# Kernel optimization log

Measured on AMD Instinct MI355X. Metric: run time of the kernel, lower is better.

The kernel has to match this reference:

```python
import jax, jax.numpy as jnp
import numpy as np

N_NODES = 100000
N_EDGES = 800000
N_GRAPHS = 64
N_ETYPES = 4
D = 150
HID = 512
PASSES = 5


def setup_inputs() -> dict:
    key = jax.random.key(0)
    ks = jax.random.split(key, 16)
    s = 0.1
    return {
        "nodes": jax.random.normal(ks[0], (N_NODES, D), jnp.float32),
        "problem_class": jax.random.normal(ks[1], (N_GRAPHS, 1), jnp.float32),
        "edge_src": jax.random.randint(ks[2], (N_EDGES,), 0, N_NODES, jnp.int32),
        "edge_dst": jax.random.randint(ks[3], (N_EDGES,), 0, N_NODES, jnp.int32),
        "edge_type": jax.random.randint(ks[4], (N_EDGES,), 0, N_ETYPES, jnp.int32),
        "graph_ids": jnp.sort(jax.random.randint(ks[5], (N_NODES,), 0, N_GRAPHS, jnp.int32)),
        "W_e": jax.random.normal(ks[6], (N_ETYPES, D, D), jnp.float32) * s,
        "b_e": jax.random.normal(ks[7], (N_ETYPES, D), jnp.float32) * s,
        "w_ih": jax.random.normal(ks[8], (3 * D, D), jnp.float32) * s,
        "w_hh": jax.random.normal(ks[9], (3 * D, D), jnp.float32) * s,
        "b_ih": jax.random.normal(ks[10], (3 * D,), jnp.float32) * s,
        "b_hh": jax.random.normal(ks[11], (3 * D,), jnp.float32) * s,
        "fc1_w": jax.random.normal(ks[12], (D + 1, HID), jnp.float32) * s,
        "fc1_b": jax.random.normal(ks[13], (HID,), jnp.float32) * s,
        "fc2_w": jax.random.normal(ks[14], (HID, 10), jnp.float32) * s,
        "fc2_b": jax.random.normal(ks[15], (10,), jnp.float32) * s,
    }


def _gru_cell(x, h, w_ih, w_hh, b_ih, b_hh):
    # torch.nn.GRUCell math, gate order (r, z, n)
    gi = x @ w_ih.T + b_ih
    gh = h @ w_hh.T + b_hh
    i_r, i_z, i_n = jnp.split(gi, 3, axis=1)
    h_r, h_z, h_n = jnp.split(gh, 3, axis=1)
    r = jax.nn.sigmoid(i_r + h_r)
    z = jax.nn.sigmoid(i_z + h_z)
    n = jnp.tanh(i_n + r * h_n)
    return (1.0 - z) * n + z * h


def reference(nodes, problem_class, edge_src, edge_dst, edge_type, graph_ids,
              W_e, b_e, w_ih, w_hh, b_ih, b_hh, fc1_w, fc1_b, fc2_w, fc2_b):
    n_nodes = nodes.shape[0]
    n_graphs = problem_class.shape[0]
    n_types = W_e.shape[0]

    # in-degree per edge type (for the per-edge Linear bias contribution)
    type_onehot = jax.nn.one_hot(edge_type, n_types, dtype=nodes.dtype)  # [E, T]
    deg = jax.ops.segment_sum(type_onehot, edge_dst, num_segments=n_nodes)  # [N, T]
    bias_inc = deg @ b_e  # [N, D] = sum_t deg_t * b_t

    h = nodes
    for _ in range(PASSES):
        h_src = h[edge_src]  # [E, D] gather
        inc = bias_inc
        for t in range(n_types):
            # aggregate first, apply the edge-type Linear after (linearity)
            agg = jax.ops.segment_sum(
                jnp.where((edge_type == t)[:, None], h_src, 0.0),
                edge_dst, num_segments=n_nodes)  # [N, D]
            inc = inc + agg @ W_e[t].T
        h = _gru_cell(inc, h, w_ih, w_hh, b_ih, b_hh)

    # graph readout: sum nodes, log, nan -> 0, relu
    g = jax.ops.segment_sum(h, graph_ids, num_segments=n_graphs)  # [B, D]
    l = jnp.log(g)
    l = jax.nn.relu(jnp.where(jnp.isnan(l), 0.0, l))
    x = jnp.concatenate([l, problem_class], axis=1)  # [B, D+1]
    x = jax.nn.leaky_relu(x @ fc1_w + fc1_b)
    return x @ fc2_w + fc2_b
```

## Files before the change

kernel.cpp:

```cpp
#include <hip/hip_runtime.h>
#include <hip/hip_bf16.h>
#include <cstdint>
#include <cstddef>

#define NN 100000
#define NE 800000
#define NG 64
#define NT 4
#define DD 150
#define HS 160
#define HIDN 512
#define NPASS 5
#define NBINS (NN*NT)
#define RPB 16

typedef short  s8v  __attribute__((ext_vector_type(8)));
typedef float  f32x4 __attribute__((ext_vector_type(4)));

static __device__ __forceinline__ float sigmoidf_(float x){ return 1.f/(1.f+expf(-x)); }
static __device__ __forceinline__ short f2bf(float x){
  __hip_bfloat16 b = __float2bfloat16(x);
  return *(short*)&b;
}
static __device__ __forceinline__ float bf2f(short s){
  union { unsigned u; float f; } v; v.u = ((unsigned)(unsigned short)s) << 16; return v.f;
}
static __device__ __forceinline__ void split_bf(float x, short& hi, short& lo){
  hi = f2bf(x);
  lo = f2bf(x - bf2f(hi));
}


__global__ void count_kernel(const int* __restrict__ dst, const int* __restrict__ typ,
                             unsigned* __restrict__ deg){
  int e = blockIdx.x*256 + threadIdx.x;
  if (e < NE) atomicAdd(&deg[dst[e]*NT + typ[e]], 1u);
}

__device__ unsigned block_excl_base(unsigned threadSum){
  const int tid = threadIdx.x;
  const int lane = tid & 63, wid = tid >> 6;
  unsigned s = threadSum;
  #pragma unroll
  for (int d = 1; d < 64; d <<= 1){ unsigned t = __shfl_up(s, d); if (lane >= d) s += t; }
  __shared__ unsigned wsum[4];
  if (lane == 63) wsum[wid] = s;
  __syncthreads();
  unsigned base = 0;
  for (int w = 0; w < wid; w++) base += wsum[w];
  return base + s - threadSum;
}

__global__ void scan_reduce(const unsigned* __restrict__ deg, unsigned* __restrict__ bsum){
  const int base = blockIdx.x*1024 + threadIdx.x*4;
  unsigned s = 0;
  #pragma unroll
  for (int i = 0; i < 4; i++){ const int idx = base+i; if (idx < NBINS) s += deg[idx]; }
  #pragma unroll
  for (int d = 1; d < 64; d <<= 1) s += __shfl_down(s, d);
  __shared__ unsigned ws4[4];
  const int lane = threadIdx.x & 63, wid = threadIdx.x >> 6;
  if (lane == 0) ws4[wid] = s;
  __syncthreads();
  if (threadIdx.x == 0) bsum[blockIdx.x] = ws4[0]+ws4[1]+ws4[2]+ws4[3];
}

__global__ void scan_block(unsigned* bsum, int n){
  const int tid = threadIdx.x;
  unsigned v[4]; unsigned s = 0;
  #pragma unroll
  for (int i = 0; i < 4; i++){ const int idx = tid*4+i; v[i] = (idx < n) ? bsum[idx] : 0u; s += v[i]; }
  unsigned run = block_excl_base(s);
  #pragma unroll
  for (int i = 0; i < 4; i++){ const int idx = tid*4+i; if (idx < n) bsum[idx] = run; run += v[i]; }
}

__global__ void scan_final(const unsigned* __restrict__ deg, const unsigned* __restrict__ bsum,
                           unsigned* __restrict__ off){
  const int tid = threadIdx.x;
  const int base0 = blockIdx.x*1024 + tid*4;
  unsigned v[4]; unsigned s = 0;
  #pragma unroll
  for (int i = 0; i < 4; i++){ const int idx = base0+i; v[i] = (idx < NBINS) ? deg[idx] : 0u; s += v[i]; }
  unsigned run = block_excl_base(s) + bsum[blockIdx.x];
  #pragma unroll
  for (int i = 0; i < 4; i++){ const int idx = base0+i; if (idx < NBINS) off[idx] = run; run += v[i]; }
  if (blockIdx.x == 0 && tid == 0) off[NBINS] = NE;
}

__global__ void scatter_sort(const int* __restrict__ src, const int* __restrict__ dst,
                             const int* __restrict__ typ, unsigned* __restrict__ cur,
                             int* __restrict__ srcSorted){
  int e = blockIdx.x*256 + threadIdx.x;
  if (e < NE){
    const int bin = dst[e]*NT + typ[e];
    const unsigned p = atomicAdd(&cur[bin], 1u);
    srcSorted[p] = src[e];
  }
}

__global__ void init_h(const float* __restrict__ nodes, float* __restrict__ h0){
  const long long idx = (long long)blockIdx.x*256 + threadIdx.x;
  if (idx >= (long long)NN*HS) return;
  const int row = (int)(idx / HS), col = (int)(idx % HS);
  float v = 0.f;
  if (col < DD) v = nodes[(size_t)row*DD + col];
  h0[idx] = v;
}

__global__ void build_bfrag_msg(const float* __restrict__ W, unsigned short* __restrict__ out){
  const int idx = blockIdx.x*256 + threadIdx.x;
  if (idx >= NT*5*10*2*512) return;
  const int w = idx & 511;
  int r = idx >> 9;
  const int c = r % 2;  r /= 2;
  const int i = r % 10; r /= 10;
  const int s = r % 5;  const int t = r / 5;
  const int l = w >> 3, j = w & 7;
  const int n  = 16*i + (l & 15);
  const int kk = 32*s + (l >> 4)*8 + j;
  float v = 0.f;
  if (n < DD && kk < DD) v = W[(size_t)(t*DD + n)*DD + kk];
  short hi, lo; split_bf(v, hi, lo);
  out[(size_t)((t*5 + s)*20 + i*2 + c)*512 + w] = (unsigned short)(c ? lo : hi);
}

__global__ void build_bfrag_gru(const float* __restrict__ w_ih, const float* __restrict__ w_hh,
                                unsigned short* __restrict__ out){
  const int idx = blockIdx.x*256 + threadIdx.x;
  if (idx >= 10*3*2*2*5*512) return;
  const int w = idx & 511;
  int r = idx >> 9;
  const int s = r % 5;    r /= 5;
  const int c = r % 2;    r /= 2;
  const int u = r % 2;    r /= 2;
  const int part = r % 3; const int iT = r / 3;
  const int P = part*2 + u;
  const int g = P >> 1;
  const float* W = (P & 1) ? w_hh : w_ih;
  const int l = w >> 3, j = w & 7;
  const int n  = 16*iT + (l & 15);
  const int kk = 32*s + (l >> 4)*8 + j;
  float v = 0.f;
  if (n < DD && kk < DD) v = W[(size_t)(g*DD + n)*DD + kk];
  short hi, lo; split_bf(v, hi, lo);
  out[(size_t)((iT*3 + part)*20 + u*10 + c*5 + s)*512 + w] = (unsigned short)(c ? lo : hi);
}

#define MFMA3(acc, ahi, alo, bhi, blo) \
  acc = __builtin_amdgcn_mfma_f32_16x16x32_bf16(ahi, bhi, acc, 0,0,0); \
  acc = __builtin_amdgcn_mfma_f32_16x16x32_bf16(alo, bhi, acc, 0,0,0); \
  acc = __builtin_amdgcn_mfma_f32_16x16x32_bf16(ahi, blo, acc, 0,0,0);

__global__ __launch_bounds__(256, 2) void msg_kernel(
    const float* __restrict__ h, const int* __restrict__ srcS,
    const unsigned* __restrict__ off, const unsigned* __restrict__ deg,
    const float* __restrict__ b_e,
    const unsigned short* __restrict__ BfE2,
    float* __restrict__ inc)
{
  __shared__ short Bs[2][20*512];
  const int tid = threadIdx.x, wave = tid >> 6, l = tid & 63;
  const int m = l & 15, q = l >> 4, q8 = q*8;
  const int arow = blockIdx.x*64 + wave*16 + m;
  const bool av = (arow < NN);
  const int lb8 = l*8;

  f32x4 acc[10];
  #pragma unroll
  for (int i = 0; i < 10; i++) acc[i] = (f32x4)(0.0f);

  #pragma unroll
  for (int k2 = 0; k2 < 5; k2++){
    const int c = tid + k2*256;
    *(s8v*)(&Bs[0][c*8]) = *(const s8v*)(BfE2 + (size_t)c*8);
  }
  __syncthreads();

  s8v sv[5];
  for (int t = 0; t < NT; t++){
    #pragma unroll
    for (int k2 = 0; k2 < 5; k2++){
      const int c = tid + k2*256;
      sv[k2] = *(const s8v*)(BfE2 + (size_t)(t*5 + 1)*10240 + (size_t)c*8);
    }

    float a[5][8];
    #pragma unroll
    for (int s = 0; s < 5; s++)
      #pragma unroll
      for (int j = 0; j < 8; j++) a[s][j] = 0.f;

    int lo = 0, hi = 0;
    if (av){ const int bin = arow*NT + t; lo = (int)off[bin]; hi = (int)off[bin+1]; }
    int e = lo;
    int i0 = (e   < hi) ? srcS[e]   : 0;
    int i1 = (e+1 < hi) ? srcS[e+1] : -1;
    while (e < hi){
      const int n0 = (e+2 < hi) ? srcS[e+2] : 0;
      const int n1 = (e+3 < hi) ? srcS[e+3] : -1;
      const float* p0 = h + (size_t)i0*HS + q8;
      const float* p1 = h + (size_t)(i1 < 0 ? 0 : i1)*HS + q8;
      const float w1 = (i1 < 0) ? 0.f : 1.f;
      f32x4 v[10], u[10];
      #pragma unroll
      for (int s = 0; s < 5; s++){
        v[2*s]   = *(const f32x4*)(p0 + 32*s);
        v[2*s+1] = *(const f32x4*)(p0 + 32*s + 4);
      }
      #pragma unroll
      for (int s = 0; s < 5; s++){
        u[2*s]   = *(const f32x4*)(p1 + 32*s);
        u[2*s+1] = *(const f32x4*)(p1 + 32*s + 4);
      }
      #pragma unroll
      for (int s = 0; s < 5; s++){
        #pragma unroll
        for (int j = 0; j < 4; j++){
          a[s][j]   += v[2*s][j];
          a[s][j]   = fmaf(w1, u[2*s][j], a[s][j]);
          a[s][4+j] += v[2*s+1][j];
          a[s][4+j] = fmaf(w1, u[2*s+1][j], a[s][4+j]);
        }
      }
      e += 2; i0 = n0; i1 = n1;
    }

    s8v af_hi[5], af_lo[5];
    #pragma unroll
    for (int s = 0; s < 5; s++)
      #pragma unroll
      for (int j = 0; j < 8; j++){
        short h2, l2; split_bf(a[s][j], h2, l2);
        af_hi[s][j] = h2; af_lo[s][j] = l2;
      }

    #pragma unroll
    for (int st = 0; st < 5; st++){
      const int sidx = t*5 + st;
      const short* bsr = &Bs[sidx & 1][0];
      #pragma unroll
      for (int i = 0; i < 10; i++){
        const s8v bh = *(const s8v*)(bsr + (i*2+0)*512 + lb8);
        const s8v bl = *(const s8v*)(bsr + (i*2+1)*512 + lb8);
        MFMA3(acc[i], af_hi[st], af_lo[st], bh, bl)
      }
      if (sidx + 1 < 20){
        short* bsw = &Bs[(sidx+1) & 1][0];
        #pragma unroll
        for (int k2 = 0; k2 < 5; k2++){
          const int c = tid + k2*256;
          *(s8v*)(bsw + c*8) = sv[k2];
        }
      }
      if (st < 4 && sidx + 2 < 20){
        #pragma unroll
        for (int k2 = 0; k2 < 5; k2++){
          const int c = tid + k2*256;
          sv[k2] = *(const s8v*)(BfE2 + (size_t)(sidx+2)*10240 + (size_t)c*8);
        }
      }
      __syncthreads();
    }
  }

  const int crow0 = blockIdx.x*64 + wave*16 + q*4;
  #pragma unroll
  for (int r = 0; r < 4; r++){
    const int crow = crow0 + r;
    if (crow < NN){
      const uint4 dg = *(const uint4*)(&deg[crow*NT]);
      const float d0=(float)dg.x, d1=(float)dg.y, d2=(float)dg.z, d3=(float)dg.w;
      float* op = inc + (size_t)crow*HS;
      #pragma unroll
      for (int i = 0; i < 10; i++){
        const int c = 16*i + m;
        float val = 0.f;
        if (c < DD)
          val = acc[i][r] + fmaf(d0, b_e[c], fmaf(d1, b_e[DD+c],
                  fmaf(d2, b_e[2*DD+c], d3*b_e[3*DD+c])));
        op[c] = val;
      }
    }
  }
}

__global__ __launch_bounds__(512, 2) void gru_kernel(
    const float* __restrict__ h, float* __restrict__ incnext,
    const unsigned short* __restrict__ BfG,
    const float* __restrict__ b_ih, const float* __restrict__ b_hh)
{
  __shared__ short Bs[2][20*512];
  const int tid = threadIdx.x, wave = tid >> 6, l = tid & 63;
  const int m = l & 15, q = l >> 4, q8 = q*8;
  const int arow = blockIdx.x*128 + wave*16 + m;
  const bool av = (arow < NN);
  const int lb8 = l*8;
  const int crow0 = blockIdx.x*128 + wave*16 + q*4;

  s8v afi_h[5], afi_l[5], afh_h[5], afh_l[5];
  {
    const float* ip = incnext + (size_t)(av ? arow : 0)*HS;
    const float* hp = h       + (size_t)(av ? arow : 0)*HS;
    #pragma unroll
    for (int s = 0; s < 5; s++){
      const int b = 32*s + q8;
      const f32x4 x0 = *(const f32x4*)(ip + b), x1 = *(const f32x4*)(ip + b + 4);
      const f32x4 y0 = *(const f32x4*)(hp + b), y1 = *(const f32x4*)(hp + b + 4);
      #pragma unroll
      for (int j = 0; j < 4; j++){
        short h2, l2;
        split_bf(x0[j], h2, l2); afi_h[s][j]   = h2; afi_l[s][j]   = l2;
        split_bf(x1[j], h2, l2); afi_h[s][4+j] = h2; afi_l[s][4+j] = l2;
        split_bf(y0[j], h2, l2); afh_h[s][j]   = h2; afh_l[s][j]   = l2;
        split_bf(y1[j], h2, l2); afh_h[s][4+j] = h2; afh_l[s][4+j] = l2;
      }
    }
  }

  #pragma unroll
  for (int k2 = 0; k2 < 3; k2++){
    const int c = tid + k2*512;
    if (c < 1280) *(s8v*)(&Bs[0][c*8]) = *(const s8v*)(BfG + (size_t)c*8);
  }
  __syncthreads();

  s8v sv[3];
  #pragma unroll
  for (int k2 = 0; k2 < 3; k2++){
    const int c = tid + k2*512;
    if (c < 1280) sv[k2] = *(const s8v*)(BfG + (size_t)10240 + (size_t)c*8);
  }

  f32x4 aR=(f32x4)(0.f), aZ=(f32x4)(0.f), aIN=(f32x4)(0.f), aHN=(f32x4)(0.f);
  float hv[4] = {0.f,0.f,0.f,0.f};

  for (int k = 0; k < 30; k++){
    const int iT = k/3, part = k - 3*iT;
    const int d = 16*iT + m;
    if (part == 0){
      aR = (f32x4)(0.f); aZ = (f32x4)(0.f); aIN = (f32x4)(0.f); aHN = (f32x4)(0.f);
      #pragma unroll
      for (int r = 0; r < 4; r++){
        hv[r] = 0.f;
        if (crow0 + r < NN && d < DD) hv[r] = h[(size_t)(crow0+r)*HS + d];
      }
    }

    const short* bsr = &Bs[k & 1][0];
    #pragma unroll
    for (int s = 0; s < 5; s++){
      const s8v b0h = *(const s8v*)(bsr + (     s)*512 + lb8);
      const s8v b0l = *(const s8v*)(bsr + ( 5 + s)*512 + lb8);
      const s8v b1h = *(const s8v*)(bsr + (10 + s)*512 + lb8);
      const s8v b1l = *(const s8v*)(bsr + (15 + s)*512 + lb8);
      if (part == 0){
        MFMA3(aR, afi_h[s], afi_l[s], b0h, b0l)
        MFMA3(aR, afh_h[s], afh_l[s], b1h, b1l)
      } else if (part == 1){
        MFMA3(aZ, afi_h[s], afi_l[s], b0h, b0l)
        MFMA3(aZ, afh_h[s], afh_l[s], b1h, b1l)
      } else {
        MFMA3(aIN, afi_h[s], afi_l[s], b0h, b0l)
        MFMA3(aHN, afh_h[s], afh_l[s], b1h, b1l)
      }
    }

    if (k < 29){
      short* bsw = &Bs[(k+1) & 1][0];
      #pragma unroll
      for (int k2 = 0; k2 < 3; k2++){
        const int c = tid + k2*512;
        if (c < 1280) *(s8v*)(bsw + c*8) = sv[k2];
      }
    }
    if (k < 28){
      #pragma unroll
      for (int k2 = 0; k2 < 3; k2++){
        const int c = tid + k2*512;
        if (c < 1280) sv[k2] = *(const s8v*)(BfG + (size_t)(k+2)*10240 + (size_t)c*8);
      }
    }

    if (part == 2 && d < DD){
      const float br   = b_ih[d]    + b_hh[d];
      const float bz   = b_ih[DD+d] + b_hh[DD+d];
      const float bin2 = b_ih[2*DD+d];
      const float bhn  = b_hh[2*DD+d];
      #pragma unroll
      for (int r = 0; r < 4; r++){
        const int crow = crow0 + r;
        if (crow < NN){
          const float rr = sigmoidf_(aR[r] + br);
          const float zz = sigmoidf_(aZ[r] + bz);
          const float nn = tanhf(aIN[r] + bin2 + rr*(aHN[r] + bhn));
          incnext[(size_t)crow*HS + d] = (1.f - zz)*nn + zz*hv[r];
        }
      }
    }
    __syncthreads();
  }
}

__global__ void readout1(const float* __restrict__ h, const int* __restrict__ gids,
                         float* __restrict__ part){
  const int g = blockIdx.x >> 4, s = blockIdx.x & (RPB-1);
  const int tid = threadIdx.x;
  __shared__ int sb[2];
  if (tid < 2){
    const int target = g + tid;
    int lo = 0, hi = NN;
    while (lo < hi){ const int mid = (lo+hi) >> 1; if (gids[mid] < target) lo = mid+1; else hi = mid; }
    sb[tid] = lo;
  }
  __syncthreads();
  const int lo = sb[0], hi = sb[1];
  const int len = hi - lo;
  const int per = (len + RPB - 1) / RPB;
  const int nlo = lo + s*per;
  const int nhi = (nlo + per < hi) ? (nlo + per) : hi;
  if (tid < DD){
    float acc = 0.f;
    for (int n = nlo; n < nhi; n++) acc += h[(size_t)n*HS + tid];
    part[(size_t)blockIdx.x*DD + tid] = acc;
  }
}

__global__ void readout2(const float* __restrict__ part, const float* __restrict__ pclass,
                         float* __restrict__ xbuf){
  const int g = blockIdx.x, tid = threadIdx.x;
  if (tid < DD){
    float acc = 0.f;
    #pragma unroll
    for (int s = 0; s < RPB; s++) acc += part[(size_t)(g*RPB + s)*DD + tid];
    float l = logf(acc);
    if (isnan(l)) l = 0.f;
    l = fmaxf(l, 0.f);
    xbuf[g*(DD+1)+tid] = l;
  }
  if (tid == DD) xbuf[g*(DD+1)+DD] = pclass[g];
}

__global__ void fc1_kernel(const float* __restrict__ xbuf, const float* __restrict__ w,
                           const float* __restrict__ b, float* __restrict__ hid){
  const int g = blockIdx.x, tid = threadIdx.x;
  __shared__ float xs[DD+1];
  if (tid < DD+1) xs[tid] = xbuf[g*(DD+1)+tid];
  __syncthreads();
  float acc = b[tid];
  for (int k = 0; k < DD+1; k++) acc = fmaf(xs[k], w[k*HIDN + tid], acc);
  hid[g*HIDN + tid] = (acc > 0.f) ? acc : 0.01f*acc;
}

__global__ void fc2_kernel(const float* __restrict__ hid, const float* __restrict__ w,
                           const float* __restrict__ b, float* __restrict__ out){
  const int g = blockIdx.x, tid = threadIdx.x;
  __shared__ float hs[HIDN];
  for (int i = tid; i < HIDN; i += 64) hs[i] = hid[g*HIDN + i];
  __syncthreads();
  if (tid < 10){
    float acc = b[tid];
    for (int k = 0; k < HIDN; k++) acc = fmaf(hs[k], w[k*10 + tid], acc);
    out[g*10 + tid] = acc;
  }
}

extern "C" void kernel_launch(void* const* d_in, const int* in_sizes, int n_in,
                              void* d_out, int out_size, void* d_ws, size_t ws_size,
                              hipStream_t stream)
{
  (void)in_sizes; (void)n_in; (void)out_size; (void)ws_size;
  const float* nodes  = (const float*)d_in[0];
  const float* pclass = (const float*)d_in[1];
  const int*   esrc   = (const int*)d_in[2];
  const int*   edst   = (const int*)d_in[3];
  const int*   etyp   = (const int*)d_in[4];
  const int*   gids   = (const int*)d_in[5];
  const float* W_e    = (const float*)d_in[6];
  const float* b_e    = (const float*)d_in[7];
  const float* w_ih   = (const float*)d_in[8];
  const float* w_hh   = (const float*)d_in[9];
  const float* b_ih   = (const float*)d_in[10];
  const float* b_hh   = (const float*)d_in[11];
  const float* fc1w   = (const float*)d_in[12];
  const float* fc1b   = (const float*)d_in[13];
  const float* fc2w   = (const float*)d_in[14];
  const float* fc2b   = (const float*)d_in[15];
  float* out = (float*)d_out;

  char* p = (char*)d_ws;
  auto alloc = [&](size_t bytes)->char* {
    char* r = p; p += ((bytes + 255) & ~(size_t)255); return r;
  };
  float*    h0   = (float*)alloc((size_t)NN*HS*4);
  float*    h1   = (float*)alloc((size_t)NN*HS*4);
  unsigned* deg  = (unsigned*)alloc((size_t)NBINS*4);
  unsigned* off  = (unsigned*)alloc((size_t)(NBINS+1)*4);
  unsigned* cur  = (unsigned*)alloc((size_t)NBINS*4);
  unsigned* bsum = (unsigned*)alloc(4096);
  int*      srcS = (int*)alloc((size_t)NE*4);
  unsigned short* BfE2 = (unsigned short*)alloc((size_t)20*20*512*2);
  unsigned short* BfG  = (unsigned short*)alloc((size_t)30*20*512*2);
  float*    part = (float*)alloc((size_t)NG*RPB*DD*4);
  float*    xbuf = (float*)alloc((size_t)NG*(DD+1)*4);
  float*    hidb = (float*)alloc((size_t)NG*HIDN*4);

  hipMemsetAsync(deg, 0, (size_t)NBINS*4, stream);
  count_kernel<<<(NE+255)/256, 256, 0, stream>>>(edst, etyp, deg);
  const int SCB = (NBINS + 1023)/1024;
  scan_reduce<<<SCB, 256, 0, stream>>>(deg, bsum);
  scan_block<<<1, 256, 0, stream>>>(bsum, SCB);
  scan_final<<<SCB, 256, 0, stream>>>(deg, bsum, off);
  hipMemcpyAsync(cur, off, (size_t)NBINS*4, hipMemcpyDeviceToDevice, stream);
  scatter_sort<<<(NE+255)/256, 256, 0, stream>>>(esrc, edst, etyp, cur, srcS);
  build_bfrag_msg<<<(NT*5*10*2*512+255)/256, 256, 0, stream>>>(W_e, BfE2);
  build_bfrag_gru<<<(10*3*2*2*5*512+255)/256, 256, 0, stream>>>(w_ih, w_hh, BfG);
  init_h<<<(int)(((long long)NN*HS + 255)/256), 256, 0, stream>>>(nodes, h0);

  float* hb[2] = {h0, h1};
  const int growsM = (NN + 63)/64;
  const int growsG = (NN + 127)/128;
  for (int pass = 0; pass < NPASS; pass++){
    const float* hc = hb[pass & 1];
    float*       hn = hb[(pass + 1) & 1];
    msg_kernel<<<growsM, 256, 0, stream>>>(hc, srcS, off, deg, b_e, BfE2, hn);
    gru_kernel<<<growsG, 512, 0, stream>>>(hc, hn, BfG, b_ih, b_hh);
  }

  readout1<<<NG*RPB, 256, 0, stream>>>(hb[NPASS & 1], gids, part);
  readout2<<<NG, 256, 0, stream>>>(part, pclass, xbuf);
  fc1_kernel<<<NG, HIDN, 0, stream>>>(xbuf, fc1w, fc1b, hidb);
  fc2_kernel<<<NG, 64, 0, stream>>>(hidb, fc2w, fc2b, out);
}
```

Before: 2.220 ms.

## Shrink GRU blocks to 256 threads and use per-step temporary accumulators

The GRU kernel now runs 64 rows per block with 256 threads instead of 128 rows with 512, so each block copies the shared weight tiles with 5 loads per thread rather than 3. The four persistent gate accumulators are replaced by two temporaries per step, which removes the per-part branching around the MFMAs and cuts register use. The goal is higher occupancy and simpler inner-loop code. The cost is that each weight tile is now loaded from global memory by twice as many blocks.

```diff
diff --git a/kernel.cpp b/kernel.cpp
--- a/kernel.cpp
+++ b/kernel.cpp
@@ -285,7 +285,7 @@
   }
 }
 
-__global__ __launch_bounds__(512, 2) void gru_kernel(
+__global__ __launch_bounds__(256, 2) void gru_kernel(
     const float* __restrict__ h, float* __restrict__ incnext,
     const unsigned short* __restrict__ BfG,
     const float* __restrict__ b_ih, const float* __restrict__ b_hh)
@@ -293,10 +293,10 @@
   __shared__ short Bs[2][20*512];
   const int tid = threadIdx.x, wave = tid >> 6, l = tid & 63;
   const int m = l & 15, q = l >> 4, q8 = q*8;
-  const int arow = blockIdx.x*128 + wave*16 + m;
+  const int arow = blockIdx.x*64 + wave*16 + m;
   const bool av = (arow < NN);
   const int lb8 = l*8;
-  const int crow0 = blockIdx.x*128 + wave*16 + q*4;
+  const int crow0 = blockIdx.x*64 + wave*16 + q*4;
 
   s8v afi_h[5], afi_l[5], afh_h[5], afh_l[5];
   {
@@ -319,27 +319,26 @@
   }
 
   #pragma unroll
-  for (int k2 = 0; k2 < 3; k2++){
-    const int c = tid + k2*512;
-    if (c < 1280) *(s8v*)(&Bs[0][c*8]) = *(const s8v*)(BfG + (size_t)c*8);
-  }
-  __syncthreads();
-
-  s8v sv[3];
-  #pragma unroll
-  for (int k2 = 0; k2 < 3; k2++){
-    const int c = tid + k2*512;
-    if (c < 1280) sv[k2] = *(const s8v*)(BfG + (size_t)10240 + (size_t)c*8);
-  }
-
-  f32x4 aR=(f32x4)(0.f), aZ=(f32x4)(0.f), aIN=(f32x4)(0.f), aHN=(f32x4)(0.f);
+  for (int k2 = 0; k2 < 5; k2++){
+    const int c = tid + k2*256;
+    *(s8v*)(&Bs[0][c*8]) = *(const s8v*)(BfG + (size_t)c*8);
+  }
+  __syncthreads();
+
+  s8v sv[5];
+  #pragma unroll
+  for (int k2 = 0; k2 < 5; k2++){
+    const int c = tid + k2*256;
+    sv[k2] = *(const s8v*)(BfG + (size_t)10240 + (size_t)c*8);
+  }
+
+  f32x4 aR=(f32x4)(0.f), aZ=(f32x4)(0.f);
   float hv[4] = {0.f,0.f,0.f,0.f};
 
   for (int k = 0; k < 30; k++){
     const int iT = k/3, part = k - 3*iT;
     const int d = 16*iT + m;
     if (part == 0){
-      aR = (f32x4)(0.f); aZ = (f32x4)(0.f); aIN = (f32x4)(0.f); aHN = (f32x4)(0.f);
       #pragma unroll
       for (int r = 0; r < 4; r++){
         hv[r] = 0.f;
@@ -348,41 +347,38 @@
     }
 
     const short* bsr = &Bs[k & 1][0];
+    f32x4 tI = (f32x4)(0.f), tH = (f32x4)(0.f);
     #pragma unroll
     for (int s = 0; s < 5; s++){
       const s8v b0h = *(const s8v*)(bsr + (     s)*512 + lb8);
       const s8v b0l = *(const s8v*)(bsr + ( 5 + s)*512 + lb8);
       const s8v b1h = *(const s8v*)(bsr + (10 + s)*512 + lb8);
       const s8v b1l = *(const s8v*)(bsr + (15 + s)*512 + lb8);
-      if (part == 0){
-        MFMA3(aR, afi_h[s], afi_l[s], b0h, b0l)
-        MFMA3(aR, afh_h[s], afh_l[s], b1h, b1l)
-      } else if (part == 1){
-        MFMA3(aZ, afi_h[s], afi_l[s], b0h, b0l)
-        MFMA3(aZ, afh_h[s], afh_l[s], b1h, b1l)
-      } else {
-        MFMA3(aIN, afi_h[s], afi_l[s], b0h, b0l)
-        MFMA3(aHN, afh_h[s], afh_l[s], b1h, b1l)
-      }
+      MFMA3(tI, afi_h[s], afi_l[s], b0h, b0l)
+      MFMA3(tH, afh_h[s], afh_l[s], b1h, b1l)
     }
 
     if (k < 29){
       short* bsw = &Bs[(k+1) & 1][0];
       #pragma unroll
-      for (int k2 = 0; k2 < 3; k2++){
-        const int c = tid + k2*512;
-        if (c < 1280) *(s8v*)(bsw + c*8) = sv[k2];
+      for (int k2 = 0; k2 < 5; k2++){
+        const int c = tid + k2*256;
+        *(s8v*)(bsw + c*8) = sv[k2];
       }
     }
     if (k < 28){
       #pragma unroll
-      for (int k2 = 0; k2 < 3; k2++){
-        const int c = tid + k2*512;
-        if (c < 1280) sv[k2] = *(const s8v*)(BfG + (size_t)(k+2)*10240 + (size_t)c*8);
-      }
-    }
-
-    if (part == 2 && d < DD){
+      for (int k2 = 0; k2 < 5; k2++){
+        const int c = tid + k2*256;
+        sv[k2] = *(const s8v*)(BfG + (size_t)(k+2)*10240 + (size_t)c*8);
+      }
+    }
+
+    if (part == 0){
+      aR = tI + tH;
+    } else if (part == 1){
+      aZ = tI + tH;
+    } else if (d < DD){
       const float br   = b_ih[d]    + b_hh[d];
       const float bz   = b_ih[DD+d] + b_hh[DD+d];
       const float bin2 = b_ih[2*DD+d];
@@ -393,7 +389,7 @@
         if (crow < NN){
           const float rr = sigmoidf_(aR[r] + br);
           const float zz = sigmoidf_(aZ[r] + bz);
-          const float nn = tanhf(aIN[r] + bin2 + rr*(aHN[r] + bhn));
+          const float nn = tanhf(tI[r] + bin2 + rr*(tH[r] + bhn));
           incnext[(size_t)crow*HS + d] = (1.f - zz)*nn + zz*hv[r];
         }
       }
@@ -518,13 +514,12 @@
   init_h<<<(int)(((long long)NN*HS + 255)/256), 256, 0, stream>>>(nodes, h0);
 
   float* hb[2] = {h0, h1};
-  const int growsM = (NN + 63)/64;
-  const int growsG = (NN + 127)/128;
+  const int grows = (NN + 63)/64;
   for (int pass = 0; pass < NPASS; pass++){
     const float* hc = hb[pass & 1];
     float*       hn = hb[(pass + 1) & 1];
-    msg_kernel<<<growsM, 256, 0, stream>>>(hc, srcS, off, deg, b_e, BfE2, hn);
-    gru_kernel<<<growsG, 512, 0, stream>>>(hc, hn, BfG, b_ih, b_hh);
+    msg_kernel<<<grows, 256, 0, stream>>>(hc, srcS, off, deg, b_e, BfE2, hn);
+    gru_kernel<<<grows, 256, 0, stream>>>(hc, hn, BfG, b_ih, b_hh);
   }
 
   readout1<<<NG*RPB, 256, 0, stream>>>(hb[NPASS & 1], gids, part);
```

After: 1.848 ms. 1.2x faster.
